# Kernel optimization log

Measured on AMD Instinct MI355X. Metric: run time of the kernel, lower is better.

## Reference

```python
import jax, jax.numpy as jnp
import numpy as np


def setup_inputs() -> dict:
    key = jax.random.key(0)
    k1, k2, k3, k4, k5 = jax.random.split(key, 5)
    B, S, H, NL = 256, 128, 768, 2
    return {
        "t_logits": jax.random.normal(k1, (B, NL), dtype=jnp.float32),
        "s_logits": jax.random.normal(k2, (B, NL), dtype=jnp.float32),
        "t_features": jax.random.normal(k3, (B, S, H), dtype=jnp.float32),
        "s_features": jax.random.normal(k4, (B, S, H), dtype=jnp.float32),
        "labels": jax.random.randint(k5, (B,), 0, NL, dtype=jnp.int64),
        "k": 5,
        "temperature": 4,
    }


def reference(t_logits, s_logits, t_features, s_features, labels, k, temperature):
    B = s_features.shape[0]
    D = s_features.shape[1] * s_features.shape[2]  # flattened feature dim S*H
    T = jnp.asarray(temperature, dtype=s_logits.dtype)

    # train_loss: standard cross-entropy computed inside the student model
    logp = jax.nn.log_softmax(s_logits, axis=-1)
    train_loss = -jnp.mean(jnp.take_along_axis(logp, labels[:, None].astype(jnp.int32), axis=1))

    # soft_loss: KL(batchmean) between temperature-softened teacher/student
    soft_targets = jax.nn.softmax(t_logits / T, axis=-1)
    log_probs = jax.nn.log_softmax(s_logits / T, axis=-1)
    soft_loss = jnp.sum(soft_targets * (jnp.log(soft_targets) - log_probs)) / B * T * T

    # distill_loss: per-sample squared distances to label-matched teacher
    # features, take k nearest (self included, dist 0), sum of per-neighbor
    # MSE = sqdist / D.
    tf = t_features.reshape(B, -1)
    sf = s_features.reshape(B, -1)
    # ||s_i - t_j||^2 via GEMM: [B, B]
    sq = (jnp.sum(sf * sf, axis=1)[:, None]
          + jnp.sum(tf * tf, axis=1)[None, :]
          - 2.0 * sf @ tf.T)
    sq = jnp.maximum(sq, 0.0)
    same = labels[:, None] == labels[None, :]
    masked = jnp.where(same, sq, jnp.inf)
    neg_top, _ = jax.lax.top_k(-masked, k)  # k smallest distances per row
    vals = -neg_top
    valid = jnp.isfinite(vals)  # handles groups smaller than k
    distill_loss = jnp.sum(jnp.where(valid, vals, 0.0)) / D

    return train_loss, soft_loss, distill_loss
```

## Files before the change

kernel.cpp:

```cpp
#include <hip/hip_runtime.h>
#include <math.h>


#define BM 128
#define BN 128
#define BK 32
#define LPITCH 40

typedef __attribute__((ext_vector_type(8))) short short8;
typedef __attribute__((ext_vector_type(4))) float f32x4;

__device__ inline unsigned pack_bf16(float a, float b) {
    unsigned ua = __float_as_uint(a), ub = __float_as_uint(b);
    ua = (ua + 0x7fffu + ((ua >> 16) & 1u)) >> 16;
    ub = (ub + 0x7fffu + ((ub >> 16) & 1u)) >> 16;
    return (ua & 0xffffu) | (ub << 16);
}

__global__ __launch_bounds__(256) void gemm_dot_kernel(const float* __restrict__ S,
                                                       const float* __restrict__ T,
                                                       float* __restrict__ part,
                                                       float* __restrict__ spart,
                                                       float* __restrict__ tpart,
                                                       int B, int K, int KC) {
    __shared__ __align__(16) unsigned short As[BM * LPITCH];
    __shared__ __align__(16) unsigned short Bs[BN * LPITCH];

    const int tid  = threadIdx.x;
    const int i0   = blockIdx.x * BM;
    const int j0   = blockIdx.y * BN;
    const int bz   = blockIdx.z;
    const int kbeg = bz * KC;
    const int kend = kbeg + KC;

    const int lane = tid & 63;
    const int wid  = tid >> 6;
    const int wm   = wid >> 1;
    const int wn   = wid & 1;
    const int l15  = lane & 15;
    const int quad = lane >> 4;

    const int kq4 = (tid & 7) * 4;
    int rowl[4];
    bool vi[4], vj[4];
    const float* pS[4];
    const float* pT[4];
    #pragma unroll
    for (int l = 0; l < 4; ++l) {
        rowl[l] = (l * 256 + tid) >> 3;
        int gi = i0 + rowl[l];
        int gj = j0 + rowl[l];
        vi[l] = gi < B;
        vj[l] = gj < B;
        if (gi >= B) gi = B - 1;
        if (gj >= B) gj = B - 1;
        pS[l] = S + (size_t)gi * K + kq4;
        pT[l] = T + (size_t)gj * K + kq4;
    }

    f32x4 acc[4][4] = {};
    float pn_s[4] = {0.f, 0.f, 0.f, 0.f};
    float pn_t[4] = {0.f, 0.f, 0.f, 0.f};

    float4 sv[4], tv[4];
    #pragma unroll
    for (int l = 0; l < 4; ++l) {
        sv[l] = *(const float4*)(pS[l] + kbeg);
        tv[l] = *(const float4*)(pT[l] + kbeg);
    }

    for (int kb = kbeg; kb < kend; kb += BK) {
        __syncthreads();
        #pragma unroll
        for (int l = 0; l < 4; ++l) {
            pn_s[l] += sv[l].x * sv[l].x + sv[l].y * sv[l].y
                     + sv[l].z * sv[l].z + sv[l].w * sv[l].w;
            pn_t[l] += tv[l].x * tv[l].x + tv[l].y * tv[l].y
                     + tv[l].z * tv[l].z + tv[l].w * tv[l].w;
            *(uint2*)&As[rowl[l] * LPITCH + kq4] =
                make_uint2(pack_bf16(sv[l].x, sv[l].y), pack_bf16(sv[l].z, sv[l].w));
            *(uint2*)&Bs[rowl[l] * LPITCH + kq4] =
                make_uint2(pack_bf16(tv[l].x, tv[l].y), pack_bf16(tv[l].z, tv[l].w));
        }
        const int kn = kb + BK;
        if (kn < kend) {
            #pragma unroll
            for (int l = 0; l < 4; ++l) {
                sv[l] = *(const float4*)(pS[l] + kn);
                tv[l] = *(const float4*)(pT[l] + kn);
            }
        }
        __syncthreads();

        short8 af[4], bf[4];
        #pragma unroll
        for (int mi = 0; mi < 4; ++mi)
            af[mi] = *(const short8*)&As[(wm * 64 + mi * 16 + l15) * LPITCH + quad * 8];
        #pragma unroll
        for (int ni = 0; ni < 4; ++ni)
            bf[ni] = *(const short8*)&Bs[(wn * 64 + ni * 16 + l15) * LPITCH + quad * 8];
        #pragma unroll
        for (int mi = 0; mi < 4; ++mi)
            #pragma unroll
            for (int ni = 0; ni < 4; ++ni)
                acc[mi][ni] = __builtin_amdgcn_mfma_f32_16x16x32_bf16(
                    af[mi], bf[ni], acc[mi][ni], 0, 0, 0);
    }

    float* outp = part + (size_t)bz * B * B;
    #pragma unroll
    for (int mi = 0; mi < 4; ++mi) {
        #pragma unroll
        for (int ni = 0; ni < 4; ++ni) {
            #pragma unroll
            for (int r = 0; r < 4; ++r) {
                const int ig = i0 + wm * 64 + mi * 16 + quad * 4 + r;
                const int jg = j0 + wn * 64 + ni * 16 + l15;
                if (ig < B && jg < B)
                    outp[(size_t)ig * B + jg] = acc[mi][ni][r];
            }
        }
    }

    if (blockIdx.y == 0) {
        #pragma unroll
        for (int l = 0; l < 4; ++l) {
            float v = pn_s[l];
            v += __shfl_xor(v, 1, 64);
            v += __shfl_xor(v, 2, 64);
            v += __shfl_xor(v, 4, 64);
            const int gi = i0 + rowl[l];
            if ((tid & 7) == 0 && vi[l]) spart[(size_t)bz * B + gi] = v;
        }
    }
    if (blockIdx.x == 0) {
        #pragma unroll
        for (int l = 0; l < 4; ++l) {
            float v = pn_t[l];
            v += __shfl_xor(v, 1, 64);
            v += __shfl_xor(v, 2, 64);
            v += __shfl_xor(v, 4, 64);
            const int gj = j0 + rowl[l];
            if ((tid & 7) == 0 && vj[l]) tpart[(size_t)bz * B + gj] = v;
        }
    }
}

__global__ __launch_bounds__(256) void tail_kernel(const float* __restrict__ part,
                                                   const float* __restrict__ spart,
                                                   const float* __restrict__ tpart,
                                                   const float* __restrict__ t_logits,
                                                   const float* __restrict__ s_logits,
                                                   const int* __restrict__ labels,
                                                   const int* __restrict__ kp,
                                                   const int* __restrict__ tp,
                                                   float* __restrict__ rowsum,
                                                   int* __restrict__ counter,
                                                   float* __restrict__ out,
                                                   int B, int K, int NL, int gz) {
    const int i   = blockIdx.x;
    const int tid = threadIdx.x;
    const size_t BB = (size_t)B * B;

    __shared__ float svals[256];
    __shared__ float rv[256];
    __shared__ int   ri[256];
    __shared__ float red[4];
    __shared__ int   lastf;

    float dt = 0.f, tn = 0.f;
    if (tid < B) {
        for (int z = 0; z < gz; ++z) {
            dt += part[(size_t)z * BB + (size_t)i * B + tid];
            tn += tpart[(size_t)z * B + tid];
        }
    }
    float sp = (tid < gz) ? spart[(size_t)tid * B + i] : 0.f;
    #pragma unroll
    for (int off = 32; off > 0; off >>= 1) sp += __shfl_down(sp, off, 64);
    if ((tid & 63) == 0) red[tid >> 6] = sp;
    __syncthreads();
    const float sn = red[0] + red[1] + red[2] + red[3];

    float v = INFINITY;
    if (tid < B && labels[i] == labels[tid])
        v = fmaxf(sn + tn - 2.0f * dt, 0.0f);
    svals[tid] = v;
    __syncthreads();

    const int k = kp[0];
    float sum = 0.0f;
    for (int it = 0; it < k; ++it) {
        rv[tid] = svals[tid];
        ri[tid] = tid;
        __syncthreads();
        #pragma unroll
        for (int s = 128; s > 0; s >>= 1) {
            if (tid < s) {
                if (rv[tid + s] < rv[tid]) { rv[tid] = rv[tid + s]; ri[tid] = ri[tid + s]; }
            }
            __syncthreads();
        }
        if (tid == 0) {
            if (rv[0] < 3.0e38f) sum += rv[0];
            svals[ri[0]] = INFINITY;
        }
        __syncthreads();
    }

    if (tid == 0) {
        rowsum[i] = sum;
        __threadfence();
        lastf = (atomicAdd(counter, 1) == B - 1) ? 1 : 0;
    }
    __syncthreads();
    if (!lastf) return;

    __threadfence();
    const float Tv = (float)tp[0];
    float rs = (tid < B) ? rowsum[tid] : 0.f;
    float ce = 0.0f, kl = 0.0f;
    for (int s = tid; s < B; s += 256) {
        const float* sl = s_logits + (size_t)s * NL;
        const float* tl = t_logits + (size_t)s * NL;
        float mx = -INFINITY;
        for (int c = 0; c < NL; ++c) mx = fmaxf(mx, sl[c]);
        float se = 0.0f;
        for (int c = 0; c < NL; ++c) se += expf(sl[c] - mx);
        ce += logf(se) + mx - sl[labels[s]];

        float mxs = -INFINITY, mxt = -INFINITY;
        for (int c = 0; c < NL; ++c) {
            mxs = fmaxf(mxs, sl[c] / Tv);
            mxt = fmaxf(mxt, tl[c] / Tv);
        }
        float ses = 0.0f, set = 0.0f;
        for (int c = 0; c < NL; ++c) {
            ses += expf(sl[c] / Tv - mxs);
            set += expf(tl[c] / Tv - mxt);
        }
        float lses = logf(ses) + mxs;
        float lset = logf(set) + mxt;
        for (int c = 0; c < NL; ++c) {
            float lst = tl[c] / Tv - lset;
            float ls  = sl[c] / Tv - lses;
            kl += expf(lst) * (lst - ls);
        }
    }
    #pragma unroll
    for (int off = 32; off > 0; off >>= 1) {
        ce += __shfl_down(ce, off, 64);
        kl += __shfl_down(kl, off, 64);
        rs += __shfl_down(rs, off, 64);
    }
    __shared__ float wce[4], wkl[4], wrs[4];
    if ((tid & 63) == 0) { wce[tid >> 6] = ce; wkl[tid >> 6] = kl; wrs[tid >> 6] = rs; }
    __syncthreads();
    if (tid == 0) {
        out[0] = (wce[0] + wce[1] + wce[2] + wce[3]) / (float)B;
        out[1] = (wkl[0] + wkl[1] + wkl[2] + wkl[3]) / (float)B * Tv * Tv;
        out[2] = (wrs[0] + wrs[1] + wrs[2] + wrs[3]) / (float)K;
    }
}

extern "C" void kernel_launch(void* const* d_in, const int* in_sizes, int n_in,
                              void* d_out, int out_size, void* d_ws, size_t ws_size,
                              hipStream_t stream) {
    const float* t_logits = (const float*)d_in[0];
    const float* s_logits = (const float*)d_in[1];
    const float* t_feat   = (const float*)d_in[2];
    const float* s_feat   = (const float*)d_in[3];
    const int*   labels   = (const int*)d_in[4];
    const int*   kp       = (const int*)d_in[5];
    const int*   tp       = (const int*)d_in[6];
    float* out = (float*)d_out;

    const int B  = in_sizes[4];
    const int NL = in_sizes[0] / B;
    const int K  = in_sizes[2] / B;
    const size_t BB = (size_t)B * B;

    const size_t avail = ws_size / 4;
    const int cands[] = {192, 128, 96, 64, 48, 32, 24, 16, 12, 8, 6, 4, 3, 2, 1};
    int gz = 1;
    for (int ci = 0; ci < 15; ++ci) {
        const int g = cands[ci];
        if (K % (g * BK) != 0) continue;
        const size_t need = (size_t)g * BB + 2 * (size_t)g * B + B + 4;
        if (need <= avail) { gz = g; break; }
    }
    const int KC = K / gz;

    float* ws     = (float*)d_ws;
    float* part   = ws;
    float* spart  = part + (size_t)gz * BB;
    float* tpart  = spart + (size_t)gz * B;
    float* rowsum = tpart + (size_t)gz * B;
    int*   counter = (int*)(rowsum + B);

    hipMemsetAsync(counter, 0, sizeof(int), stream);

    dim3 grid((B + BM - 1) / BM, (B + BN - 1) / BN, gz);
    gemm_dot_kernel<<<grid, 256, 0, stream>>>(s_feat, t_feat, part, spart, tpart,
                                              B, K, KC);

    tail_kernel<<<B, 256, 0, stream>>>(part, spart, tpart, t_logits, s_logits,
                                       labels, kp, tp, rowsum, counter, out,
                                       B, K, NL, gz);
}
```

Baseline: 312.1 us.

## Double BK with swizzled LDS, add split-K partial reduction kernels

Raises the K tile to 64 with two register-staged halves, and XOR-style swizzles the LDS layout to avoid bank conflicts. It restructures the split-K reduction: a separate parallel reduce kernel collapses the gz partial GEMM outputs into NS slices, and a small kernel computes the norms. This removes the serial per-row gz loop from the tail kernel. The cost is extra kernel launches and another pass over the workspace.

New measurement: 355.9 us. 14.0% more time.

```diff
diff --git a/kernel.cpp b/kernel.cpp
--- a/kernel.cpp
+++ b/kernel.cpp
@@ -4,8 +4,9 @@
 
 #define BM 128
 #define BN 128
-#define BK 32
-#define LPITCH 40
+#define BK 64
+#define LPITCH 72
+#define NS 8
 
 typedef __attribute__((ext_vector_type(8))) short short8;
 typedef __attribute__((ext_vector_type(4))) float f32x4;
@@ -40,14 +41,16 @@
     const int l15  = lane & 15;
     const int quad = lane >> 4;
 
-    const int kq4 = (tid & 7) * 4;
+    const int kq  = tid & 7;
+    const int kq4 = kq * 4;
     int rowl[4];
     bool vi[4], vj[4];
     const float* pS[4];
     const float* pT[4];
+    int woff[4][2];
     #pragma unroll
     for (int l = 0; l < 4; ++l) {
-        rowl[l] = (l * 256 + tid) >> 3;
+        rowl[l] = l * 32 + (tid >> 3);
         int gi = i0 + rowl[l];
         int gj = j0 + rowl[l];
         vi[l] = gi < B;
@@ -56,55 +59,89 @@
         if (gj >= B) gj = B - 1;
         pS[l] = S + (size_t)gi * K + kq4;
         pT[l] = T + (size_t)gj * K + kq4;
+        #pragma unroll
+        for (int h = 0; h < 2; ++h) {
+            const int g  = h * 4 + (kq >> 1);
+            const int gp = (g + 2 * (rowl[l] & 7)) & 7;
+            woff[l][h] = rowl[l] * LPITCH + gp * 8 + (kq & 1) * 4;
+        }
+    }
+    int coff[2];
+    #pragma unroll
+    for (int h = 0; h < 2; ++h)
+        coff[h] = ((h * 4 + quad + 2 * (l15 & 7)) & 7) * 8;
+    int arow[4], brow[4];
+    #pragma unroll
+    for (int t = 0; t < 4; ++t) {
+        arow[t] = (wm * 64 + t * 16 + l15) * LPITCH;
+        brow[t] = (wn * 64 + t * 16 + l15) * LPITCH;
     }
 
     f32x4 acc[4][4] = {};
     float pn_s[4] = {0.f, 0.f, 0.f, 0.f};
     float pn_t[4] = {0.f, 0.f, 0.f, 0.f};
 
-    float4 sv[4], tv[4];
+    float4 sv0[4], tv0[4], sv1[4], tv1[4];
     #pragma unroll
     for (int l = 0; l < 4; ++l) {
-        sv[l] = *(const float4*)(pS[l] + kbeg);
-        tv[l] = *(const float4*)(pT[l] + kbeg);
+        sv0[l] = *(const float4*)(pS[l] + kbeg);
+        tv0[l] = *(const float4*)(pT[l] + kbeg);
+        sv1[l] = *(const float4*)(pS[l] + kbeg + 32);
+        tv1[l] = *(const float4*)(pT[l] + kbeg + 32);
     }
 
     for (int kb = kbeg; kb < kend; kb += BK) {
         __syncthreads();
         #pragma unroll
         for (int l = 0; l < 4; ++l) {
-            pn_s[l] += sv[l].x * sv[l].x + sv[l].y * sv[l].y
-                     + sv[l].z * sv[l].z + sv[l].w * sv[l].w;
-            pn_t[l] += tv[l].x * tv[l].x + tv[l].y * tv[l].y
-                     + tv[l].z * tv[l].z + tv[l].w * tv[l].w;
-            *(uint2*)&As[rowl[l] * LPITCH + kq4] =
-                make_uint2(pack_bf16(sv[l].x, sv[l].y), pack_bf16(sv[l].z, sv[l].w));
-            *(uint2*)&Bs[rowl[l] * LPITCH + kq4] =
-                make_uint2(pack_bf16(tv[l].x, tv[l].y), pack_bf16(tv[l].z, tv[l].w));
-        }
-        const int kn = kb + BK;
-        if (kn < kend) {
+            float4 s = sv0[l], t = tv0[l];
+            pn_s[l] += s.x * s.x + s.y * s.y + s.z * s.z + s.w * s.w;
+            pn_t[l] += t.x * t.x + t.y * t.y + t.z * t.z + t.w * t.w;
+            *(uint2*)&As[woff[l][0]] = make_uint2(pack_bf16(s.x, s.y), pack_bf16(s.z, s.w));
+            *(uint2*)&Bs[woff[l][0]] = make_uint2(pack_bf16(t.x, t.y), pack_bf16(t.z, t.w));
+        }
+        {
+            const int kn = (kb + BK < kend) ? (kb + BK) : kbeg;
             #pragma unroll
             for (int l = 0; l < 4; ++l) {
-                sv[l] = *(const float4*)(pS[l] + kn);
-                tv[l] = *(const float4*)(pT[l] + kn);
+                sv0[l] = *(const float4*)(pS[l] + kn);
+                tv0[l] = *(const float4*)(pT[l] + kn);
             }
         }
+        #pragma unroll
+        for (int l = 0; l < 4; ++l) {
+            float4 s = sv1[l], t = tv1[l];
+            pn_s[l] += s.x * s.x + s.y * s.y + s.z * s.z + s.w * s.w;
+            pn_t[l] += t.x * t.x + t.y * t.y + t.z * t.z + t.w * t.w;
+            *(uint2*)&As[woff[l][1]] = make_uint2(pack_bf16(s.x, s.y), pack_bf16(s.z, s.w));
+            *(uint2*)&Bs[woff[l][1]] = make_uint2(pack_bf16(t.x, t.y), pack_bf16(t.z, t.w));
+        }
+        {
+            const int kn = (kb + BK + 32 < kend) ? (kb + BK + 32) : kbeg;
+            #pragma unroll
+            for (int l = 0; l < 4; ++l) {
+                sv1[l] = *(const float4*)(pS[l] + kn);
+                tv1[l] = *(const float4*)(pT[l] + kn);
+            }
+        }
         __syncthreads();
 
-        short8 af[4], bf[4];
-        #pragma unroll
-        for (int mi = 0; mi < 4; ++mi)
-            af[mi] = *(const short8*)&As[(wm * 64 + mi * 16 + l15) * LPITCH + quad * 8];
-        #pragma unroll
-        for (int ni = 0; ni < 4; ++ni)
-            bf[ni] = *(const short8*)&Bs[(wn * 64 + ni * 16 + l15) * LPITCH + quad * 8];
-        #pragma unroll
-        for (int mi = 0; mi < 4; ++mi)
+        #pragma unroll
+        for (int h = 0; h < 2; ++h) {
+            short8 af[4], bf[4];
+            #pragma unroll
+            for (int mi = 0; mi < 4; ++mi)
+                af[mi] = *(const short8*)&As[arow[mi] + coff[h]];
             #pragma unroll
             for (int ni = 0; ni < 4; ++ni)
-                acc[mi][ni] = __builtin_amdgcn_mfma_f32_16x16x32_bf16(
-                    af[mi], bf[ni], acc[mi][ni], 0, 0, 0);
+                bf[ni] = *(const short8*)&Bs[brow[ni] + coff[h]];
+            #pragma unroll
+            for (int mi = 0; mi < 4; ++mi)
+                #pragma unroll
+                for (int ni = 0; ni < 4; ++ni)
+                    acc[mi][ni] = __builtin_amdgcn_mfma_f32_16x16x32_bf16(
+                        af[mi], bf[ni], acc[mi][ni], 0, 0, 0);
+        }
     }
 
     float* outp = part + (size_t)bz * B * B;
@@ -129,8 +166,7 @@
             v += __shfl_xor(v, 1, 64);
             v += __shfl_xor(v, 2, 64);
             v += __shfl_xor(v, 4, 64);
-            const int gi = i0 + rowl[l];
-            if ((tid & 7) == 0 && vi[l]) spart[(size_t)bz * B + gi] = v;
+            if (kq == 0 && vi[l]) spart[(size_t)bz * B + i0 + rowl[l]] = v;
         }
     }
     if (blockIdx.x == 0) {
@@ -140,15 +176,39 @@
             v += __shfl_xor(v, 1, 64);
             v += __shfl_xor(v, 2, 64);
             v += __shfl_xor(v, 4, 64);
-            const int gj = j0 + rowl[l];
-            if ((tid & 7) == 0 && vj[l]) tpart[(size_t)bz * B + gj] = v;
-        }
-    }
-}
-
-__global__ __launch_bounds__(256) void tail_kernel(const float* __restrict__ part,
-                                                   const float* __restrict__ spart,
-                                                   const float* __restrict__ tpart,
+            if (kq == 0 && vj[l]) tpart[(size_t)bz * B + j0 + rowl[l]] = v;
+        }
+    }
+}
+
+__global__ __launch_bounds__(256) void reduce_kernel(const float* __restrict__ part,
+                                                     float* __restrict__ part2,
+                                                     int n, int gz) {
+    const int idx   = blockIdx.x * 256 + threadIdx.x;
+    const int slice = blockIdx.y;
+    if (idx >= n) return;
+    float s = 0.f;
+    for (int z = slice; z < gz; z += NS)
+        s += part[(size_t)z * n + idx];
+    part2[(size_t)slice * n + idx] = s;
+}
+
+__global__ __launch_bounds__(256) void norm_reduce_kernel(const float* __restrict__ spart,
+                                                          const float* __restrict__ tpart,
+                                                          float* __restrict__ s_nrm,
+                                                          float* __restrict__ t_nrm,
+                                                          int B, int gz) {
+    const int r = threadIdx.x;
+    if (r >= B) return;
+    const float* src = blockIdx.x ? tpart : spart;
+    float s = 0.f;
+    for (int z = 0; z < gz; ++z) s += src[(size_t)z * B + r];
+    if (blockIdx.x) t_nrm[r] = s; else s_nrm[r] = s;
+}
+
+__global__ __launch_bounds__(256) void tail_kernel(const float* __restrict__ part2,
+                                                   const float* __restrict__ s_nrm,
+                                                   const float* __restrict__ t_nrm,
                                                    const float* __restrict__ t_logits,
                                                    const float* __restrict__ s_logits,
                                                    const int* __restrict__ labels,
@@ -157,7 +217,7 @@
                                                    float* __restrict__ rowsum,
                                                    int* __restrict__ counter,
                                                    float* __restrict__ out,
-                                                   int B, int K, int NL, int gz) {
+                                                   int B, int K, int NL) {
     const int i   = blockIdx.x;
     const int tid = threadIdx.x;
     const size_t BB = (size_t)B * B;
@@ -165,26 +225,16 @@
     __shared__ float svals[256];
     __shared__ float rv[256];
     __shared__ int   ri[256];
-    __shared__ float red[4];
     __shared__ int   lastf;
 
-    float dt = 0.f, tn = 0.f;
-    if (tid < B) {
-        for (int z = 0; z < gz; ++z) {
-            dt += part[(size_t)z * BB + (size_t)i * B + tid];
-            tn += tpart[(size_t)z * B + tid];
-        }
-    }
-    float sp = (tid < gz) ? spart[(size_t)tid * B + i] : 0.f;
-    #pragma unroll
-    for (int off = 32; off > 0; off >>= 1) sp += __shfl_down(sp, off, 64);
-    if ((tid & 63) == 0) red[tid >> 6] = sp;
-    __syncthreads();
-    const float sn = red[0] + red[1] + red[2] + red[3];
-
     float v = INFINITY;
-    if (tid < B && labels[i] == labels[tid])
-        v = fmaxf(sn + tn - 2.0f * dt, 0.0f);
+    if (tid < B && labels[i] == labels[tid]) {
+        float dt = 0.f;
+        #pragma unroll
+        for (int s = 0; s < NS; ++s)
+            dt += part2[(size_t)s * BB + (size_t)i * B + tid];
+        v = fmaxf(s_nrm[i] + t_nrm[tid] - 2.0f * dt, 0.0f);
+    }
     svals[tid] = v;
     __syncthreads();
 
@@ -281,21 +331,25 @@
     const size_t BB = (size_t)B * B;
 
     const size_t avail = ws_size / 4;
-    const int cands[] = {192, 128, 96, 64, 48, 32, 24, 16, 12, 8, 6, 4, 3, 2, 1};
+    const int cands[] = {256, 192, 128, 96, 64, 48, 32, 24, 16, 12, 8, 6, 4, 3, 2, 1};
     int gz = 1;
-    for (int ci = 0; ci < 15; ++ci) {
+    for (int ci = 0; ci < 16; ++ci) {
         const int g = cands[ci];
         if (K % (g * BK) != 0) continue;
-        const size_t need = (size_t)g * BB + 2 * (size_t)g * B + B + 4;
+        const size_t need = (size_t)g * BB + (size_t)NS * BB
+                          + 2 * (size_t)g * B + 3 * (size_t)B + 1;
         if (need <= avail) { gz = g; break; }
     }
     const int KC = K / gz;
 
-    float* ws     = (float*)d_ws;
-    float* part   = ws;
-    float* spart  = part + (size_t)gz * BB;
-    float* tpart  = spart + (size_t)gz * B;
-    float* rowsum = tpart + (size_t)gz * B;
+    float* ws      = (float*)d_ws;
+    float* part    = ws;
+    float* part2   = part + (size_t)gz * BB;
+    float* spart   = part2 + (size_t)NS * BB;
+    float* tpart   = spart + (size_t)gz * B;
+    float* s_nrm   = tpart + (size_t)gz * B;
+    float* t_nrm   = s_nrm + B;
+    float* rowsum  = t_nrm + B;
     int*   counter = (int*)(rowsum + B);
 
     hipMemsetAsync(counter, 0, sizeof(int), stream);
@@ -304,7 +358,12 @@
     gemm_dot_kernel<<<grid, 256, 0, stream>>>(s_feat, t_feat, part, spart, tpart,
                                               B, K, KC);
 
-    tail_kernel<<<B, 256, 0, stream>>>(part, spart, tpart, t_logits, s_logits,
+    dim3 grid2((unsigned)((BB + 255) / 256), NS);
+    reduce_kernel<<<grid2, 256, 0, stream>>>(part, part2, (int)BB, gz);
+
+    norm_reduce_kernel<<<2, 256, 0, stream>>>(spart, tpart, s_nrm, t_nrm, B, gz);
+
+    tail_kernel<<<B, 256, 0, stream>>>(part2, s_nrm, t_nrm, t_logits, s_logits,
                                        labels, kp, tp, rowsum, counter, out,
-                                       B, K, NL, gz);
-}
+                                       B, K, NL);
+}
```

## Load fp32 tiles directly to LDS asynchronously and add split-K reduce stage

Applied to the files above, without the earlier changes.

The GEMM now copies fp32 feature tiles straight into swizzled LDS with global_load_lds, replacing the register-staged bf16 packing. Conversion to bf16 happens at fragment-load time using truncation rather than round-to-nearest. Squared norms are computed from LDS. A new reduce kernel collapses the split-K partial products into NS slices before the tail, which avoids the tail's serial loop over gz. The changes trade register pressure and fp32 LDS traffic against lost prefetch overlap, since there is now a sync after each load. Truncation also adds rounding bias to the distances.

After: 277.1 us. 1.13x faster.

```diff
diff --git a/kernel.cpp b/kernel.cpp
--- a/kernel.cpp
+++ b/kernel.cpp
@@ -4,18 +4,24 @@
 
 #define BM 128
 #define BN 128
-#define BK 32
-#define LPITCH 40
+#define BKF 32
+#define NS 8
 
 typedef __attribute__((ext_vector_type(8))) short short8;
 typedef __attribute__((ext_vector_type(4))) float f32x4;
 
-__device__ inline unsigned pack_bf16(float a, float b) {
-    unsigned ua = __float_as_uint(a), ub = __float_as_uint(b);
-    ua = (ua + 0x7fffu + ((ua >> 16) & 1u)) >> 16;
-    ub = (ub + 0x7fffu + ((ub >> 16) & 1u)) >> 16;
-    return (ua & 0xffffu) | (ub << 16);
-}
+__device__ inline void async16(const float* g, float* l) {
+    __builtin_amdgcn_global_load_lds(
+        (const __attribute__((address_space(1))) void*)g,
+        (__attribute__((address_space(3))) void*)l,
+        16, 0, 0);
+}
+
+__device__ inline unsigned pack_trunc(float a, float b) {
+    return (__float_as_uint(a) >> 16) | (__float_as_uint(b) & 0xffff0000u);
+}
+
+union U8 { short8 v; unsigned u[4]; };
 
 __global__ __launch_bounds__(256) void gemm_dot_kernel(const float* __restrict__ S,
                                                        const float* __restrict__ T,
@@ -23,8 +29,8 @@
                                                        float* __restrict__ spart,
                                                        float* __restrict__ tpart,
                                                        int B, int K, int KC) {
-    __shared__ __align__(16) unsigned short As[BM * LPITCH];
-    __shared__ __align__(16) unsigned short Bs[BN * LPITCH];
+    __shared__ __align__(16) float As[BM * BKF];
+    __shared__ __align__(16) float Bs[BN * BKF];
 
     const int tid  = threadIdx.x;
     const int i0   = blockIdx.x * BM;
@@ -40,65 +46,93 @@
     const int l15  = lane & 15;
     const int quad = lane >> 4;
 
-    const int kq4 = (tid & 7) * 4;
-    int rowl[4];
-    bool vi[4], vj[4];
-    const float* pS[4];
-    const float* pT[4];
+    const int rl = lane >> 3;
+    const int p  = lane & 7;
+    const float* srcA[4];
+    const float* srcB[4];
+    float* dstA[4];
+    float* dstB[4];
     #pragma unroll
-    for (int l = 0; l < 4; ++l) {
-        rowl[l] = (l * 256 + tid) >> 3;
-        int gi = i0 + rowl[l];
-        int gj = j0 + rowl[l];
-        vi[l] = gi < B;
-        vj[l] = gj < B;
-        if (gi >= B) gi = B - 1;
-        if (gj >= B) gj = B - 1;
-        pS[l] = S + (size_t)gi * K + kq4;
-        pT[l] = T + (size_t)gj * K + kq4;
-    }
+    for (int j = 0; j < 4; ++j) {
+        const int c   = wid * 4 + j;
+        const int row = c * 8 + rl;
+        const int g   = p ^ (row & 7);
+        int gi = i0 + row; if (gi >= B) gi = B - 1;
+        int gj = j0 + row; if (gj >= B) gj = B - 1;
+        srcA[j] = S + (size_t)gi * K + kbeg + g * 4;
+        srcB[j] = T + (size_t)gj * K + kbeg + g * 4;
+        dstA[j] = &As[c * 256];
+        dstB[j] = &Bs[c * 256];
+    }
+
+    int aoff[4], boff[4];
+    #pragma unroll
+    for (int t = 0; t < 4; ++t) {
+        const int ra = wm * 64 + t * 16 + l15;
+        aoff[t] = ra * BKF + (((2 * quad) ^ (ra & 7)) * 4);
+        const int rb = wn * 64 + t * 16 + l15;
+        boff[t] = rb * BKF + (((2 * quad) ^ (rb & 7)) * 4);
+    }
+
+    const bool doS = (blockIdx.y == 0);
+    const bool doT = (blockIdx.x == 0);
+    const int  rn  = tid >> 1;
+    const int  hn  = tid & 1;
 
     f32x4 acc[4][4] = {};
-    float pn_s[4] = {0.f, 0.f, 0.f, 0.f};
-    float pn_t[4] = {0.f, 0.f, 0.f, 0.f};
-
-    float4 sv[4], tv[4];
-    #pragma unroll
-    for (int l = 0; l < 4; ++l) {
-        sv[l] = *(const float4*)(pS[l] + kbeg);
-        tv[l] = *(const float4*)(pT[l] + kbeg);
-    }
-
-    for (int kb = kbeg; kb < kend; kb += BK) {
+    float pns = 0.f, pnt = 0.f;
+
+    for (int kb = kbeg; kb < kend; kb += BKF) {
         __syncthreads();
         #pragma unroll
-        for (int l = 0; l < 4; ++l) {
-            pn_s[l] += sv[l].x * sv[l].x + sv[l].y * sv[l].y
-                     + sv[l].z * sv[l].z + sv[l].w * sv[l].w;
-            pn_t[l] += tv[l].x * tv[l].x + tv[l].y * tv[l].y
-                     + tv[l].z * tv[l].z + tv[l].w * tv[l].w;
-            *(uint2*)&As[rowl[l] * LPITCH + kq4] =
-                make_uint2(pack_bf16(sv[l].x, sv[l].y), pack_bf16(sv[l].z, sv[l].w));
-            *(uint2*)&Bs[rowl[l] * LPITCH + kq4] =
-                make_uint2(pack_bf16(tv[l].x, tv[l].y), pack_bf16(tv[l].z, tv[l].w));
-        }
-        const int kn = kb + BK;
-        if (kn < kend) {
+        for (int j = 0; j < 4; ++j) {
+            async16(srcA[j], dstA[j]);
+            async16(srcB[j], dstB[j]);
+            srcA[j] += BKF;
+            srcB[j] += BKF;
+        }
+        __syncthreads();
+
+        if (doS) {
             #pragma unroll
-            for (int l = 0; l < 4; ++l) {
-                sv[l] = *(const float4*)(pS[l] + kn);
-                tv[l] = *(const float4*)(pT[l] + kn);
-            }
-        }
-        __syncthreads();
+            for (int j = 0; j < 4; ++j) {
+                const int pos = hn * 4 + ((j + rn) & 3);
+                f32x4 v = *(const f32x4*)&As[rn * BKF + pos * 4];
+                pns += v.x * v.x + v.y * v.y + v.z * v.z + v.w * v.w;
+            }
+        }
+        if (doT) {
+            #pragma unroll
+            for (int j = 0; j < 4; ++j) {
+                const int pos = hn * 4 + ((j + rn) & 3);
+                f32x4 v = *(const f32x4*)&Bs[rn * BKF + pos * 4];
+                pnt += v.x * v.x + v.y * v.y + v.z * v.z + v.w * v.w;
+            }
+        }
 
         short8 af[4], bf[4];
         #pragma unroll
-        for (int mi = 0; mi < 4; ++mi)
-            af[mi] = *(const short8*)&As[(wm * 64 + mi * 16 + l15) * LPITCH + quad * 8];
-        #pragma unroll
-        for (int ni = 0; ni < 4; ++ni)
-            bf[ni] = *(const short8*)&Bs[(wn * 64 + ni * 16 + l15) * LPITCH + quad * 8];
+        for (int t = 0; t < 4; ++t) {
+            f32x4 va = *(const f32x4*)&As[aoff[t]];
+            f32x4 vb = *(const f32x4*)&As[aoff[t] ^ 4];
+            U8 u;
+            u.u[0] = pack_trunc(va.x, va.y);
+            u.u[1] = pack_trunc(va.z, va.w);
+            u.u[2] = pack_trunc(vb.x, vb.y);
+            u.u[3] = pack_trunc(vb.z, vb.w);
+            af[t] = u.v;
+        }
+        #pragma unroll
+        for (int t = 0; t < 4; ++t) {
+            f32x4 va = *(const f32x4*)&Bs[boff[t]];
+            f32x4 vb = *(const f32x4*)&Bs[boff[t] ^ 4];
+            U8 u;
+            u.u[0] = pack_trunc(va.x, va.y);
+            u.u[1] = pack_trunc(va.z, va.w);
+            u.u[2] = pack_trunc(vb.x, vb.y);
+            u.u[3] = pack_trunc(vb.z, vb.w);
+            bf[t] = u.v;
+        }
         #pragma unroll
         for (int mi = 0; mi < 4; ++mi)
             #pragma unroll
@@ -122,33 +156,50 @@
         }
     }
 
-    if (blockIdx.y == 0) {
-        #pragma unroll
-        for (int l = 0; l < 4; ++l) {
-            float v = pn_s[l];
-            v += __shfl_xor(v, 1, 64);
-            v += __shfl_xor(v, 2, 64);
-            v += __shfl_xor(v, 4, 64);
-            const int gi = i0 + rowl[l];
-            if ((tid & 7) == 0 && vi[l]) spart[(size_t)bz * B + gi] = v;
-        }
-    }
-    if (blockIdx.x == 0) {
-        #pragma unroll
-        for (int l = 0; l < 4; ++l) {
-            float v = pn_t[l];
-            v += __shfl_xor(v, 1, 64);
-            v += __shfl_xor(v, 2, 64);
-            v += __shfl_xor(v, 4, 64);
-            const int gj = j0 + rowl[l];
-            if ((tid & 7) == 0 && vj[l]) tpart[(size_t)bz * B + gj] = v;
-        }
-    }
-}
-
-__global__ __launch_bounds__(256) void tail_kernel(const float* __restrict__ part,
-                                                   const float* __restrict__ spart,
-                                                   const float* __restrict__ tpart,
+    if (doS) {
+        float v = pns + __shfl_xor(pns, 1, 64);
+        if (hn == 0 && i0 + rn < B) spart[(size_t)bz * B + i0 + rn] = v;
+    }
+    if (doT) {
+        float v = pnt + __shfl_xor(pnt, 1, 64);
+        if (hn == 0 && j0 + rn < B) tpart[(size_t)bz * B + j0 + rn] = v;
+    }
+}
+
+__global__ __launch_bounds__(256) void reduce_kernel(const float* __restrict__ part,
+                                                     const float* __restrict__ spart,
+                                                     const float* __restrict__ tpart,
+                                                     float* __restrict__ part2,
+                                                     float* __restrict__ snorm2,
+                                                     float* __restrict__ tnorm2,
+                                                     int n, int B, int gz) {
+    const int s  = blockIdx.y;
+    const int bx = blockIdx.x;
+    const int t  = threadIdx.x;
+    if ((int)bx * 256 < n) {
+        const int idx = bx * 256 + t;
+        if (idx < n) {
+            float a = 0.f;
+            for (int z = s; z < gz; z += NS)
+                a += part[(size_t)z * n + idx];
+            part2[(size_t)s * n + idx] = a;
+        }
+    } else {
+        if (t < B) {
+            float a = 0.f, b = 0.f;
+            for (int z = s; z < gz; z += NS) {
+                a += spart[(size_t)z * B + t];
+                b += tpart[(size_t)z * B + t];
+            }
+            snorm2[s * B + t] = a;
+            tnorm2[s * B + t] = b;
+        }
+    }
+}
+
+__global__ __launch_bounds__(256) void tail_kernel(const float* __restrict__ part2,
+                                                   const float* __restrict__ snorm2,
+                                                   const float* __restrict__ tnorm2,
                                                    const float* __restrict__ t_logits,
                                                    const float* __restrict__ s_logits,
                                                    const int* __restrict__ labels,
@@ -157,7 +208,7 @@
                                                    float* __restrict__ rowsum,
                                                    int* __restrict__ counter,
                                                    float* __restrict__ out,
-                                                   int B, int K, int NL, int gz) {
+                                                   int B, int K, int NL) {
     const int i   = blockIdx.x;
     const int tid = threadIdx.x;
     const size_t BB = (size_t)B * B;
@@ -165,26 +216,19 @@
     __shared__ float svals[256];
     __shared__ float rv[256];
     __shared__ int   ri[256];
-    __shared__ float red[4];
     __shared__ int   lastf;
 
-    float dt = 0.f, tn = 0.f;
-    if (tid < B) {
-        for (int z = 0; z < gz; ++z) {
-            dt += part[(size_t)z * BB + (size_t)i * B + tid];
-            tn += tpart[(size_t)z * B + tid];
-        }
-    }
-    float sp = (tid < gz) ? spart[(size_t)tid * B + i] : 0.f;
-    #pragma unroll
-    for (int off = 32; off > 0; off >>= 1) sp += __shfl_down(sp, off, 64);
-    if ((tid & 63) == 0) red[tid >> 6] = sp;
-    __syncthreads();
-    const float sn = red[0] + red[1] + red[2] + red[3];
-
     float v = INFINITY;
-    if (tid < B && labels[i] == labels[tid])
+    if (tid < B && labels[i] == labels[tid]) {
+        float dt = 0.f, sn = 0.f, tn = 0.f;
+        #pragma unroll
+        for (int s = 0; s < NS; ++s) {
+            dt += part2[(size_t)s * BB + (size_t)i * B + tid];
+            sn += snorm2[s * B + i];
+            tn += tnorm2[s * B + tid];
+        }
         v = fmaxf(sn + tn - 2.0f * dt, 0.0f);
+    }
     svals[tid] = v;
     __syncthreads();
 
@@ -281,21 +325,25 @@
     const size_t BB = (size_t)B * B;
 
     const size_t avail = ws_size / 4;
-    const int cands[] = {192, 128, 96, 64, 48, 32, 24, 16, 12, 8, 6, 4, 3, 2, 1};
+    const int cands[] = {192, 256, 128, 96, 64, 48, 32, 24, 16, 12, 8, 6, 4, 3, 2, 1};
     int gz = 1;
-    for (int ci = 0; ci < 15; ++ci) {
+    for (int ci = 0; ci < 16; ++ci) {
         const int g = cands[ci];
-        if (K % (g * BK) != 0) continue;
-        const size_t need = (size_t)g * BB + 2 * (size_t)g * B + B + 4;
+        if (K % (g * BKF) != 0) continue;
+        const size_t need = (size_t)g * BB + (size_t)NS * BB
+                          + 2 * (size_t)g * B + 2 * (size_t)NS * B + B + 1;
         if (need <= avail) { gz = g; break; }
     }
     const int KC = K / gz;
 
-    float* ws     = (float*)d_ws;
-    float* part   = ws;
-    float* spart  = part + (size_t)gz * BB;
-    float* tpart  = spart + (size_t)gz * B;
-    float* rowsum = tpart + (size_t)gz * B;
+    float* ws      = (float*)d_ws;
+    float* part    = ws;
+    float* part2   = part + (size_t)gz * BB;
+    float* spart   = part2 + (size_t)NS * BB;
+    float* tpart   = spart + (size_t)gz * B;
+    float* snorm2  = tpart + (size_t)gz * B;
+    float* tnorm2  = snorm2 + (size_t)NS * B;
+    float* rowsum  = tnorm2 + (size_t)NS * B;
     int*   counter = (int*)(rowsum + B);
 
     hipMemsetAsync(counter, 0, sizeof(int), stream);
@@ -304,7 +352,11 @@
     gemm_dot_kernel<<<grid, 256, 0, stream>>>(s_feat, t_feat, part, spart, tpart,
                                               B, K, KC);
 
-    tail_kernel<<<B, 256, 0, stream>>>(part, spart, tpart, t_logits, s_logits,
+    dim3 grid2((unsigned)(BB / 256 + 1), NS);
+    reduce_kernel<<<grid2, 256, 0, stream>>>(part, spart, tpart, part2,
+                                             snorm2, tnorm2, (int)BB, B, gz);
+
+    tail_kernel<<<B, 256, 0, stream>>>(part2, snorm2, tnorm2, t_logits, s_logits,
                                        labels, kp, tp, rowsum, counter, out,
-                                       B, K, NL, gz);
-}
+                                       B, K, NL);
+}
```
